# Optimization experiments

Hardware: AMD Instinct MI355X
Metric: run time of the kernel (lower is better)

## Reference

```python
import jax, jax.numpy as jnp
import numpy as np

HEADS = 16
D_MODEL = 2048
HEAD_DIM = D_MODEL // HEADS


def setup_inputs() -> dict:
    key = jax.random.key(0)
    ks = jax.random.split(key, 8)
    s = 1.0 / np.sqrt(D_MODEL)
    return {
        "hidden_states": jax.random.normal(ks[0], (2, 2048, D_MODEL), jnp.float32),
        "Wq": jax.random.normal(ks[1], (D_MODEL, D_MODEL), jnp.float32) * s,
        "bq": jax.random.normal(ks[2], (D_MODEL,), jnp.float32) * s,
        "Wk": jax.random.normal(ks[3], (D_MODEL, D_MODEL), jnp.float32) * s,
        "Wv": jax.random.normal(ks[4], (D_MODEL, D_MODEL), jnp.float32) * s,
        "bv": jax.random.normal(ks[5], (D_MODEL,), jnp.float32) * s,
        "Wo": jax.random.normal(ks[6], (D_MODEL, D_MODEL), jnp.float32) * s,
        "bo": jax.random.normal(ks[7], (D_MODEL,), jnp.float32) * s,
    }


def reference(hidden_states, Wq, bq, Wk, Wv, bv, Wo, bo):
    bsz, q_len, _ = hidden_states.shape
    # torch Linear: y = x @ W^T + b; k_W has no bias
    q = hidden_states @ Wq.T + bq
    k = hidden_states @ Wk.T
    v = hidden_states @ Wv.T + bv
    # [b, h, s, d]
    def split_heads(t):
        return t.reshape(bsz, q_len, HEADS, HEAD_DIM).transpose(0, 2, 1, 3)
    q, k, v = split_heads(q), split_heads(k), split_heads(v)
    scale = 1.0 / np.sqrt(HEAD_DIM).astype(np.float32)
    attn_weights = jnp.einsum("bhqd,bhkd->bhqk", q, k) * scale
    attn_weights = jax.nn.softmax(attn_weights, axis=-1)
    attn_output = jnp.einsum("bhqk,bhkd->bhqd", attn_weights, v)
    attn_output = attn_output.transpose(0, 2, 1, 3).reshape(bsz, q_len, D_MODEL)
    attn_output = attn_output @ Wo.T + bo
    return attn_output, attn_weights
```

## Files before the change

### kernel.cpp

```cpp
#include <hip/hip_runtime.h>

typedef _Float16 f16;
typedef _Float16 f16x4 __attribute__((ext_vector_type(4)));
typedef _Float16 f16x8 __attribute__((ext_vector_type(8)));
typedef float f32x4 __attribute__((ext_vector_type(4)));

#define DM 2048
#define NT 4096
#define SEQ 2048
#define HD 128
#define NBH 32
#define QSCALE (0.08838834764831845f * 1.4426950408889634f)

__device__ __forceinline__ void gload16(const f16* g, f16* l) {
  __builtin_amdgcn_global_load_lds(
      (const __attribute__((address_space(1))) void*)g,
      (__attribute__((address_space(3))) void*)l, 16, 0, 0);
}

__global__ __launch_bounds__(256) void cvt_f32_f16(const float* __restrict__ src,
                                                   f16* __restrict__ dst, int n4) {
  int i = blockIdx.x * 256 + threadIdx.x;
  int st = gridDim.x * 256;
  for (; i < n4; i += st) {
    float4 v = ((const float4*)src)[i];
    f16x4 h = {(f16)v.x, (f16)v.y, (f16)v.z, (f16)v.w};
    ((f16x4*)dst)[i] = h;
  }
}

__global__ __launch_bounds__(256) void cvt3_f32_f16(const float* __restrict__ s0,
                                                    const float* __restrict__ s1,
                                                    const float* __restrict__ s2,
                                                    f16* __restrict__ dst) {
  int i = blockIdx.x * 256 + threadIdx.x;
  int st = gridDim.x * 256;
  for (; i < 3 * 1048576; i += st) {
    const int r = i >> 20, j = i & 1048575;
    const float* s = (r == 0) ? s0 : ((r == 1) ? s1 : s2);
    float4 v = ((const float4*)s)[j];
    f16x4 h = {(f16)v.x, (f16)v.y, (f16)v.z, (f16)v.w};
    ((f16x4*)dst)[i] = h;
  }
}

template <int MODE>
__global__ __launch_bounds__(256, 2) void gemm_bt(const f16* __restrict__ A,
                                                  const f16* __restrict__ B,
                                                  const float* __restrict__ bias1,
                                                  const float* __restrict__ bias2,
                                                  float* __restrict__ outF,
                                                  f16* __restrict__ outQ,
                                                  f16* __restrict__ outK,
                                                  f16* __restrict__ outV) {
  __shared__ __align__(16) f16 smem[128 * 136];
  f16* const lA = smem;
  f16* const lB = smem + 8192;

  const int tid = threadIdx.x;
  const int w = tid >> 6, l = tid & 63;
  const int wr = w >> 1, wc = w & 1;

  const int nbx = gridDim.x;
  const int flat = blockIdx.y * nbx + blockIdx.x;
  const int chunk = (nbx * gridDim.y) >> 3;
  const int swz = (flat & 7) * chunk + (flat >> 3);
  const int row0 = (swz / nbx) * 128, col0 = (swz % nbx) * 128;

  f32x4 acc[4][4] = {};

  const int srow = w * 32 + (l >> 2);
  const int sk = (l & 3) * 8;
  const f16* gA = A + (size_t)(row0 + srow) * DM + sk;
  const f16* gB = B + (size_t)(col0 + srow) * DM + sk;

  {
    f16* sA = lA + w * 1024;
    f16* sB = lB + w * 1024;
    gload16(gA, sA);
    gload16(gA + 16 * DM, sA + 512);
    gload16(gB, sB);
    gload16(gB + 16 * DM, sB + 512);
  }

  int cur = 0;
  for (int k0 = 0; k0 < DM; k0 += 32) {
    __syncthreads();
    if (k0 + 32 < DM) {
      f16* sA = lA + (cur ^ 1) * 4096 + w * 1024;
      f16* sB = lB + (cur ^ 1) * 4096 + w * 1024;
      gload16(gA + k0 + 32, sA);
      gload16(gA + k0 + 32 + 16 * DM, sA + 512);
      gload16(gB + k0 + 32, sB);
      gload16(gB + k0 + 32 + 16 * DM, sB + 512);
    }
    f16x8 af[4], bf[4];
#pragma unroll
    for (int i = 0; i < 4; i++)
      af[i] = *(const f16x8*)&lA[cur * 4096 + (wr * 64 + i * 16 + (l & 15)) * 32 + (l >> 4) * 8];
#pragma unroll
    for (int i = 0; i < 4; i++)
      bf[i] = *(const f16x8*)&lB[cur * 4096 + (wc * 64 + i * 16 + (l & 15)) * 32 + (l >> 4) * 8];
#pragma unroll
    for (int mi = 0; mi < 4; mi++)
#pragma unroll
      for (int ni = 0; ni < 4; ni++)
        acc[mi][ni] = __builtin_amdgcn_mfma_f32_16x16x32_f16(af[mi], bf[ni], acc[mi][ni], 0, 0, 0);
    cur ^= 1;
  }

  const int rl0 = wr * 64 + (l >> 4) * 4;
  const int cl0 = wc * 64 + (l & 15);
  if constexpr (MODE == 0) {
#pragma unroll
    for (int mi = 0; mi < 4; mi++) {
#pragma unroll
      for (int ni = 0; ni < 4; ni++) {
        const int col = col0 + cl0 + ni * 16;
        const float bi = bias1[col];
#pragma unroll
        for (int j = 0; j < 4; j++) {
          const int row = row0 + rl0 + mi * 16 + j;
          outF[(size_t)row * DM + col] = acc[mi][ni][j] + bi;
        }
      }
    }
  } else {
    const int region = col0 >> 11;
    const int c2 = col0 & 2047;
    __syncthreads();
#pragma unroll
    for (int mi = 0; mi < 4; mi++) {
#pragma unroll
      for (int ni = 0; ni < 4; ni++) {
        const int cl = cl0 + ni * 16;
        const int cg = c2 + cl;
#pragma unroll
        for (int j = 0; j < 4; j++) {
          const int rl = rl0 + mi * 16 + j;
          const float v = acc[mi][ni][j];
          f16 hv;
          if (region == 0)
            hv = (f16)((v + bias1[cg]) * QSCALE);
          else if (region == 1)
            hv = (f16)v;
          else
            hv = (f16)(v + bias2[cg]);
          if (region == 2)
            smem[cl * 136 + rl] = hv;
          else
            smem[rl * 136 + cl] = hv;
        }
      }
    }
    __syncthreads();
    if (region == 2) {
      const int b = row0 >> 11, h = c2 >> 7, s0 = row0 & 2047;
      f16* const dst = outV + ((size_t)(b * 16 + h) * HD) * SEQ + s0;
#pragma unroll
      for (int it = 0; it < 8; it++) {
        const int ck = it * 256 + tid;
        const int rr = ck >> 4, cc = (ck & 15) * 8;
        *(f16x8*)&dst[(size_t)rr * SEQ + cc] = *(const f16x8*)&smem[rr * 136 + cc];
      }
    } else {
      f16* const dst = (region == 0 ? outQ : outK) + (size_t)row0 * DM + c2;
#pragma unroll
      for (int it = 0; it < 8; it++) {
        const int ck = it * 256 + tid;
        const int rr = ck >> 4, cc = (ck & 15) * 8;
        *(f16x8*)&dst[(size_t)rr * DM + cc] = *(const f16x8*)&smem[rr * 136 + cc];
      }
    }
  }
}

__global__ __launch_bounds__(256, 2) void attn(const f16* __restrict__ Q,
                                               const f16* __restrict__ Kt,
                                               const f16* __restrict__ Vt,
                                               float* __restrict__ Pout,
                                               f16* __restrict__ Oout) {
  __shared__ __align__(16) f16 smem[36864];
  f16* const lP = smem + 32768;

  const int tid = threadIdx.x, w = tid >> 6, l = tid & 63;
  const int t = l >> 4, sl = l & 15, t8 = l >> 3, sl8 = l & 7;

  const int flat = blockIdx.y * gridDim.x + blockIdx.x;
  const int swz = (flat & 7) * 128 + (flat >> 3);
  const int bh = swz >> 5, q0 = (swz & 31) * 64;

  const int b = bh >> 4, h = bh & 15;
  const f16* Qg = Q + (size_t)(b * SEQ) * DM + h * HD;
  const f16* Kg = Kt + (size_t)(b * SEQ) * DM + h * HD;
  const f16* Vg = Vt + (size_t)bh * HD * SEQ;

#pragma unroll
  for (int c = 0; c < 4; c++) {
    const int row = w * 16 + c * 4 + t;
    const int ch = sl ^ (row & 7);
    gload16(Qg + (size_t)(q0 + row) * DM + ch * 8, smem + 16384 + w * 2048 + c * 512);
    gload16(Kg + (size_t)row * DM + ch * 8, smem + w * 2048 + c * 512);
  }
  __syncthreads();

  f16x8 qf[4];
  {
    const int row = w * 16 + sl;
#pragma unroll
    for (int g = 0; g < 4; g++) {
      const int ch = (g * 4 + t) ^ (row & 7);
      qf[g] = *(const f16x8*)&smem[16384 + row * 128 + ch * 8];
    }
  }

  float lsum = 0.0f;

  for (int kb = 0; kb < 32; ++kb) {
    f16* const kc = smem + (kb & 1) * 8192;
    if (kb < 31) {
      f16* const kn = smem + ((kb + 1) & 1) * 8192;
#pragma unroll
      for (int c = 0; c < 4; c++) {
        const int row = w * 16 + c * 4 + t;
        const int ch = sl ^ (row & 7);
        gload16(Kg + (size_t)((kb + 1) * 64 + row) * DM + ch * 8, kn + w * 2048 + c * 512);
      }
    }
#pragma unroll
    for (int cb = 0; cb < 4; ++cb) {
      f32x4 s = {0.f, 0.f, 0.f, 0.f};
      const int key = cb * 16 + sl;
#pragma unroll
      for (int g = 0; g < 4; ++g) {
        const int ch = (g * 4 + t) ^ (key & 7);
        f16x8 kf = *(const f16x8*)&kc[key * 128 + ch * 8];
        s = __builtin_amdgcn_mfma_f32_16x16x32_f16(kf, qf[g], s, 0, 0, 0);
      }
#pragma unroll
      for (int j = 0; j < 4; j++) lsum += __builtin_amdgcn_exp2f(s[j]);
    }
    __syncthreads();
  }
  lsum += __shfl_xor(lsum, 16);
  lsum += __shfl_xor(lsum, 32);
  const float inv = 1.0f / lsum;

  {
#pragma unroll
    for (int c = 0; c < 4; c++) {
      const int row = w * 16 + c * 4 + t;
      const int ch = sl ^ (row & 7);
      gload16(Kg + (size_t)row * DM + ch * 8, smem + w * 2048 + c * 512);
    }
#pragma unroll
    for (int c = 0; c < 4; c++) {
      const int row = w * 32 + c * 8 + t8;
      const int ch = sl8 ^ (row & 7);
      gload16(Vg + (size_t)row * SEQ + ch * 8, smem + 16384 + w * 2048 + c * 512);
    }
  }
  __syncthreads();

  f32x4 oacc[8] = {};
  const int qrow = w * 16 + sl;
  float* const Prow = Pout + ((size_t)bh * SEQ + q0 + qrow) * SEQ;

  for (int kb = 0; kb < 32; ++kb) {
    f16* const kc = smem + (kb & 1) * 8192;
    f16* const vc = smem + 16384 + (kb & 1) * 8192;
    if (kb < 31) {
      f16* const kn = smem + ((kb + 1) & 1) * 8192;
      f16* const vn = smem + 16384 + ((kb + 1) & 1) * 8192;
#pragma unroll
      for (int c = 0; c < 4; c++) {
        const int row = w * 16 + c * 4 + t;
        const int ch = sl ^ (row & 7);
        gload16(Kg + (size_t)((kb + 1) * 64 + row) * DM + ch * 8, kn + w * 2048 + c * 512);
      }
#pragma unroll
      for (int c = 0; c < 4; c++) {
        const int row = w * 32 + c * 8 + t8;
        const int ch = sl8 ^ (row & 7);
        gload16(Vg + (size_t)row * SEQ + (kb + 1) * 64 + ch * 8, vn + w * 2048 + c * 512);
      }
    }
#pragma unroll
    for (int cb = 0; cb < 4; ++cb) {
      f32x4 s = {0.f, 0.f, 0.f, 0.f};
      const int key = cb * 16 + sl;
#pragma unroll
      for (int g = 0; g < 4; ++g) {
        const int ch = (g * 4 + t) ^ (key & 7);
        f16x8 kf = *(const f16x8*)&kc[key * 128 + ch * 8];
        s = __builtin_amdgcn_mfma_f32_16x16x32_f16(kf, qf[g], s, 0, 0, 0);
      }
      f32x4 p4;
      f16x4 ph;
#pragma unroll
      for (int j = 0; j < 4; j++) {
        const float p = __builtin_amdgcn_exp2f(s[j]) * inv;
        p4[j] = p;
        ph[j] = (f16)p;
      }
      __builtin_nontemporal_store(p4, (f32x4*)(Prow + kb * 64 + cb * 16 + t * 4));
      const int chs = (cb * 2 + (t >> 1)) ^ (qrow & 7);
      *(f16x4*)&lP[qrow * 64 + chs * 8 + (t & 1) * 4] = ph;
    }
    f16x8 pf[2];
#pragma unroll
    for (int ks = 0; ks < 2; ++ks) {
      const int ch = (ks * 4 + t) ^ (qrow & 7);
      pf[ks] = *(const f16x8*)&lP[qrow * 64 + ch * 8];
    }
    __builtin_amdgcn_s_setprio(1);
#pragma unroll
    for (int cb = 0; cb < 8; ++cb) {
      const int d = cb * 16 + sl;
#pragma unroll
      for (int ks = 0; ks < 2; ++ks) {
        const int ch = (ks * 4 + t) ^ (d & 7);
        f16x8 vf = *(const f16x8*)&vc[d * 64 + ch * 8];
        oacc[cb] = __builtin_amdgcn_mfma_f32_16x16x32_f16(pf[ks], vf, oacc[cb], 0, 0, 0);
      }
    }
    __builtin_amdgcn_s_setprio(0);
    __syncthreads();
  }

#pragma unroll
  for (int cb = 0; cb < 8; ++cb) {
    const int d = cb * 16 + sl;
#pragma unroll
    for (int j = 0; j < 4; j++) {
      const int lrow = w * 16 + t * 4 + j;
      Oout[((size_t)(b * SEQ + q0 + lrow)) * DM + h * HD + d] = (f16)oacc[cb][j];
    }
  }
}

extern "C" void kernel_launch(void* const* d_in, const int* in_sizes, int n_in,
                              void* d_out, int out_size, void* d_ws, size_t ws_size,
                              hipStream_t stream) {
  const float* hs = (const float*)d_in[0];
  const float* Wq = (const float*)d_in[1];
  const float* bq = (const float*)d_in[2];
  const float* Wk = (const float*)d_in[3];
  const float* Wv = (const float*)d_in[4];
  const float* bv = (const float*)d_in[5];
  const float* Wo = (const float*)d_in[6];
  const float* bo = (const float*)d_in[7];
  float* out = (float*)d_out;
  float* Pout = out + (size_t)NT * DM;

  f16* q16 = (f16*)d_ws;
  f16* k16 = q16 + (size_t)NT * DM;
  f16* vt16 = k16 + (size_t)NT * DM;
  f16* ao16 = vt16 + (size_t)NT * DM;
  f16* hs16 = (f16*)Pout;
  f16* wqkv16 = hs16 + (size_t)NT * DM;
  f16* wo16 = q16;

  cvt_f32_f16<<<2048, 256, 0, stream>>>(hs, hs16, NT * DM / 4);
  cvt3_f32_f16<<<2048, 256, 0, stream>>>(Wq, Wk, Wv, wqkv16);

  gemm_bt<3><<<dim3(6144 / 128, NT / 128), 256, 0, stream>>>(
      hs16, wqkv16, bq, bv, nullptr, q16, k16, vt16);

  attn<<<dim3(SEQ / 64, NBH), 256, 0, stream>>>(q16, k16, vt16, Pout, ao16);

  cvt_f32_f16<<<1024, 256, 0, stream>>>(Wo, wo16, DM * DM / 4);
  gemm_bt<0><<<dim3(DM / 128, NT / 128), 256, 0, stream>>>(
      ao16, wo16, bo, nullptr, out, nullptr, nullptr, nullptr);
}
```

Before: 413.7 us.

## Rewrite GEMMs as 8-wave 128x256 tiles with triple-buffered LDS pipeline

Replaces the 4-wave 128x128 GEMM with an 8-wave 128x256 tile kernel. It uses K=64 steps with a three-stage global_load_lds ring, an XOR-swizzled LDS layout to avoid bank conflicts, and explicit waitcnt, barrier and setprio scheduling that interleaves prefetch with MFMA phases. The aim is to hide global-memory latency, raise per-block reuse and cut LDS conflicts in both the QKV and output projections. In exchange it uses much more LDS (144KB per block), which may limit occupancy, and its correctness depends on hand-tuned wait counts.

Result: faster. 388.4 us (-6.1%).

```diff
diff --git a/kernel.cpp b/kernel.cpp
--- a/kernel.cpp
+++ b/kernel.cpp
@@ -17,6 +17,16 @@
       (const __attribute__((address_space(1))) void*)g,
       (__attribute__((address_space(3))) void*)l, 16, 0, 0);
 }
+
+#define LGKM0                                         \
+  asm volatile("s_waitcnt lgkmcnt(0)" ::: "memory"); \
+  __builtin_amdgcn_sched_barrier(0)
+#define VMC6                                         \
+  asm volatile("s_waitcnt vmcnt(6)" ::: "memory");   \
+  __builtin_amdgcn_sched_barrier(0)
+#define VMC0                                         \
+  asm volatile("s_waitcnt vmcnt(0)" ::: "memory");   \
+  __builtin_amdgcn_sched_barrier(0)
 
 __global__ __launch_bounds__(256) void cvt_f32_f16(const float* __restrict__ src,
                                                    f16* __restrict__ dst, int n4) {
@@ -45,72 +55,122 @@
 }
 
 template <int MODE>
-__global__ __launch_bounds__(256, 2) void gemm_bt(const f16* __restrict__ A,
-                                                  const f16* __restrict__ B,
-                                                  const float* __restrict__ bias1,
-                                                  const float* __restrict__ bias2,
-                                                  float* __restrict__ outF,
-                                                  f16* __restrict__ outQ,
-                                                  f16* __restrict__ outK,
-                                                  f16* __restrict__ outV) {
-  __shared__ __align__(16) f16 smem[128 * 136];
-  f16* const lA = smem;
-  f16* const lB = smem + 8192;
-
+__global__ __launch_bounds__(512, 2) void gemm8(const f16* __restrict__ A,
+                                                const f16* __restrict__ Bm,
+                                                const float* __restrict__ bias1,
+                                                const float* __restrict__ bias2,
+                                                float* __restrict__ outF,
+                                                f16* __restrict__ outQ,
+                                                f16* __restrict__ outK,
+                                                f16* __restrict__ outV) {
+  __shared__ __align__(16) f16 smem[73728];
   const int tid = threadIdx.x;
   const int w = tid >> 6, l = tid & 63;
-  const int wr = w >> 1, wc = w & 1;
+  const int wr = w >> 2, wc = w & 3;
+  const int sl = l & 15, t4 = l >> 4;
 
   const int nbx = gridDim.x;
   const int flat = blockIdx.y * nbx + blockIdx.x;
   const int chunk = (nbx * gridDim.y) >> 3;
   const int swz = (flat & 7) * chunk + (flat >> 3);
-  const int row0 = (swz / nbx) * 128, col0 = (swz % nbx) * 128;
+  const int row0 = (swz / nbx) * 128, col0 = (swz % nbx) * 256;
 
   f32x4 acc[4][4] = {};
 
-  const int srow = w * 32 + (l >> 2);
-  const int sk = (l & 3) * 8;
-  const f16* gA = A + (size_t)(row0 + srow) * DM + sk;
-  const f16* gB = B + (size_t)(col0 + srow) * DM + sk;
-
-  {
-    f16* sA = lA + w * 1024;
-    f16* sB = lB + w * 1024;
-    gload16(gA, sA);
-    gload16(gA + 16 * DM, sA + 512);
-    gload16(gB, sB);
-    gload16(gB + 16 * DM, sB + 512);
-  }
+  const int sr8 = l >> 3;
+  const int sch = (l & 7) ^ (sr8 & 7);
+  const f16* gA0 = A + (size_t)(row0 + w * 8 + sr8) * DM + sch * 8;
+  const f16* gB0 = Bm + (size_t)(col0 + w * 8 + sr8) * DM + sch * 8;
+
+#define SA(tb, kt, r) \
+  gload16(gA0 + (size_t)(r) * 64 * DM + (kt) * 64, smem + (tb) * 8192 + (r) * 4096 + w * 512)
+#define SB(tb, kt, r)                                  \
+  gload16(gB0 + (size_t)(r) * 64 * DM + (kt) * 64,    \
+          smem + 24576 + (tb) * 16384 + (r) * 4096 + w * 512)
+#define MF(mi, ni, av, bv) \
+  acc[mi][ni] = __builtin_amdgcn_mfma_f32_16x16x32_f16(av, bv, acc[mi][ni], 0, 0, 0)
+
+  const int sx = sl & 7;
+  const int sk0 = (t4 ^ sx) * 8;
+  const int sk1 = ((4 + t4) ^ sx) * 8;
+  const int arow = (wr * 64 + sl) * 64;
+  const int brow = (wc * 64 + sl) * 64;
+
+  SA(0, 0, 0); SA(0, 0, 1);
+  SB(0, 0, 0); SB(0, 0, 1); SB(0, 0, 2); SB(0, 0, 3);
+  SA(1, 1, 0); SA(1, 1, 1);
+  SB(1, 1, 0); SB(1, 1, 1); SB(1, 1, 2); SB(1, 1, 3);
+  VMC6;
+  __builtin_amdgcn_s_barrier();
 
   int cur = 0;
-  for (int k0 = 0; k0 < DM; k0 += 32) {
-    __syncthreads();
-    if (k0 + 32 < DM) {
-      f16* sA = lA + (cur ^ 1) * 4096 + w * 1024;
-      f16* sB = lB + (cur ^ 1) * 4096 + w * 1024;
-      gload16(gA + k0 + 32, sA);
-      gload16(gA + k0 + 32 + 16 * DM, sA + 512);
-      gload16(gB + k0 + 32, sB);
-      gload16(gB + k0 + 32 + 16 * DM, sB + 512);
-    }
-    f16x8 af[4], bf[4];
-#pragma unroll
-    for (int i = 0; i < 4; i++)
-      af[i] = *(const f16x8*)&lA[cur * 4096 + (wr * 64 + i * 16 + (l & 15)) * 32 + (l >> 4) * 8];
-#pragma unroll
-    for (int i = 0; i < 4; i++)
-      bf[i] = *(const f16x8*)&lB[cur * 4096 + (wc * 64 + i * 16 + (l & 15)) * 32 + (l >> 4) * 8];
-#pragma unroll
-    for (int mi = 0; mi < 4; mi++)
-#pragma unroll
-      for (int ni = 0; ni < 4; ni++)
-        acc[mi][ni] = __builtin_amdgcn_mfma_f32_16x16x32_f16(af[mi], bf[ni], acc[mi][ni], 0, 0, 0);
-    cur ^= 1;
-  }
-
-  const int rl0 = wr * 64 + (l >> 4) * 4;
-  const int cl0 = wc * 64 + (l & 15);
+#pragma unroll 1
+  for (int t = 0; t < 32; ++t) {
+    const int nb = (cur == 0) ? 2 : cur - 1;
+    const bool pf = (t + 2 < 32);
+    const int ab = cur * 8192;
+    const int bb = 24576 + cur * 16384;
+    f16x8 b0, b1, b2, b3, a0, a1;
+
+    b0 = *(const f16x8*)&smem[bb + brow + sk0];
+    b1 = *(const f16x8*)&smem[bb + brow + 1024 + sk0];
+    b2 = *(const f16x8*)&smem[bb + brow + 2048 + sk0];
+    b3 = *(const f16x8*)&smem[bb + brow + 3072 + sk0];
+    a0 = *(const f16x8*)&smem[ab + arow + sk0];
+    a1 = *(const f16x8*)&smem[ab + arow + 1024 + sk0];
+    if (pf) { SA(nb, t + 2, 0); SA(nb, t + 2, 1); }
+    __builtin_amdgcn_s_barrier();
+    LGKM0;
+    __builtin_amdgcn_s_setprio(1);
+    MF(0, 0, a0, b0); MF(0, 1, a0, b1); MF(0, 2, a0, b2); MF(0, 3, a0, b3);
+    MF(1, 0, a1, b0); MF(1, 1, a1, b1); MF(1, 2, a1, b2); MF(1, 3, a1, b3);
+    __builtin_amdgcn_s_setprio(0);
+    __builtin_amdgcn_s_barrier();
+
+    a0 = *(const f16x8*)&smem[ab + arow + 2048 + sk0];
+    a1 = *(const f16x8*)&smem[ab + arow + 3072 + sk0];
+    if (pf) { SB(nb, t + 2, 0); SB(nb, t + 2, 1); }
+    __builtin_amdgcn_s_barrier();
+    LGKM0;
+    __builtin_amdgcn_s_setprio(1);
+    MF(2, 0, a0, b0); MF(2, 1, a0, b1); MF(2, 2, a0, b2); MF(2, 3, a0, b3);
+    MF(3, 0, a1, b0); MF(3, 1, a1, b1); MF(3, 2, a1, b2); MF(3, 3, a1, b3);
+    __builtin_amdgcn_s_setprio(0);
+    __builtin_amdgcn_s_barrier();
+
+    b0 = *(const f16x8*)&smem[bb + brow + sk1];
+    b1 = *(const f16x8*)&smem[bb + brow + 1024 + sk1];
+    b2 = *(const f16x8*)&smem[bb + brow + 2048 + sk1];
+    b3 = *(const f16x8*)&smem[bb + brow + 3072 + sk1];
+    a0 = *(const f16x8*)&smem[ab + arow + sk1];
+    a1 = *(const f16x8*)&smem[ab + arow + 1024 + sk1];
+    if (pf) { SB(nb, t + 2, 2); SB(nb, t + 2, 3); }
+    __builtin_amdgcn_s_barrier();
+    LGKM0;
+    __builtin_amdgcn_s_setprio(1);
+    MF(0, 0, a0, b0); MF(0, 1, a0, b1); MF(0, 2, a0, b2); MF(0, 3, a0, b3);
+    MF(1, 0, a1, b0); MF(1, 1, a1, b1); MF(1, 2, a1, b2); MF(1, 3, a1, b3);
+    __builtin_amdgcn_s_setprio(0);
+    __builtin_amdgcn_s_barrier();
+
+    a0 = *(const f16x8*)&smem[ab + arow + 2048 + sk1];
+    a1 = *(const f16x8*)&smem[ab + arow + 3072 + sk1];
+    __builtin_amdgcn_s_barrier();
+    LGKM0;
+    __builtin_amdgcn_s_setprio(1);
+    MF(2, 0, a0, b0); MF(2, 1, a0, b1); MF(2, 2, a0, b2); MF(2, 3, a0, b3);
+    MF(3, 0, a1, b0); MF(3, 1, a1, b1); MF(3, 2, a1, b2); MF(3, 3, a1, b3);
+    __builtin_amdgcn_s_setprio(0);
+    if (t < 30) { VMC6; } else { VMC0; }
+    __builtin_amdgcn_s_barrier();
+    cur = (cur == 2) ? 0 : cur + 1;
+  }
+#undef SA
+#undef SB
+#undef MF
+
+  const int rl0 = wr * 64 + t4 * 4;
+  const int cl0 = wc * 64 + sl;
   if constexpr (MODE == 0) {
 #pragma unroll
     for (int mi = 0; mi < 4; mi++) {
@@ -129,47 +189,49 @@
     const int region = col0 >> 11;
     const int c2 = col0 & 2047;
     __syncthreads();
-#pragma unroll
-    for (int mi = 0; mi < 4; mi++) {
-#pragma unroll
-      for (int ni = 0; ni < 4; ni++) {
-        const int cl = cl0 + ni * 16;
-        const int cg = c2 + cl;
-#pragma unroll
-        for (int j = 0; j < 4; j++) {
-          const int rl = rl0 + mi * 16 + j;
-          const float v = acc[mi][ni][j];
-          f16 hv;
-          if (region == 0)
-            hv = (f16)((v + bias1[cg]) * QSCALE);
-          else if (region == 1)
-            hv = (f16)v;
-          else
-            hv = (f16)(v + bias2[cg]);
-          if (region == 2)
-            smem[cl * 136 + rl] = hv;
-          else
-            smem[rl * 136 + cl] = hv;
+    if (region == 2) {
+#pragma unroll
+      for (int mi = 0; mi < 4; mi++)
+#pragma unroll
+        for (int ni = 0; ni < 4; ni++) {
+          const int cl = cl0 + ni * 16;
+          const float bb2 = bias2[c2 + cl];
+#pragma unroll
+          for (int j = 0; j < 4; j++)
+            smem[cl * 136 + rl0 + mi * 16 + j] = (f16)(acc[mi][ni][j] + bb2);
         }
-      }
-    }
-    __syncthreads();
-    if (region == 2) {
-      const int b = row0 >> 11, h = c2 >> 7, s0 = row0 & 2047;
-      f16* const dst = outV + ((size_t)(b * 16 + h) * HD) * SEQ + s0;
-#pragma unroll
-      for (int it = 0; it < 8; it++) {
-        const int ck = it * 256 + tid;
-        const int rr = ck >> 4, cc = (ck & 15) * 8;
-        *(f16x8*)&dst[(size_t)rr * SEQ + cc] = *(const f16x8*)&smem[rr * 136 + cc];
+      __syncthreads();
+      const int b = row0 >> 11, s0 = row0 & 2047;
+#pragma unroll
+      for (int it = 0; it < 8; ++it) {
+        const int ck = it * 512 + tid;
+        const int ci = ck >> 4, cc = (ck & 15) * 8;
+        const int dg = c2 + ci;
+        *(f16x8*)&outV[((size_t)(b * 16 + (dg >> 7)) * HD + (dg & 127)) * SEQ + s0 + cc] =
+            *(const f16x8*)&smem[ci * 136 + cc];
       }
     } else {
+#pragma unroll
+      for (int mi = 0; mi < 4; mi++)
+#pragma unroll
+        for (int ni = 0; ni < 4; ni++) {
+          const int cl = cl0 + ni * 16;
+          const int cg = c2 + cl;
+          const float badd = (region == 0) ? bias1[cg] : 0.0f;
+#pragma unroll
+          for (int j = 0; j < 4; j++) {
+            float v = acc[mi][ni][j] + badd;
+            if (region == 0) v *= QSCALE;
+            smem[(rl0 + mi * 16 + j) * 264 + cl] = (f16)v;
+          }
+        }
+      __syncthreads();
       f16* const dst = (region == 0 ? outQ : outK) + (size_t)row0 * DM + c2;
 #pragma unroll
-      for (int it = 0; it < 8; it++) {
-        const int ck = it * 256 + tid;
-        const int rr = ck >> 4, cc = (ck & 15) * 8;
-        *(f16x8*)&dst[(size_t)rr * DM + cc] = *(const f16x8*)&smem[rr * 136 + cc];
+      for (int it = 0; it < 8; ++it) {
+        const int ck = it * 512 + tid;
+        const int rr = ck >> 5, cc = (ck & 31) * 8;
+        *(f16x8*)&dst[(size_t)rr * DM + cc] = *(const f16x8*)&smem[rr * 264 + cc];
       }
     }
   }
@@ -364,12 +426,12 @@
   cvt_f32_f16<<<2048, 256, 0, stream>>>(hs, hs16, NT * DM / 4);
   cvt3_f32_f16<<<2048, 256, 0, stream>>>(Wq, Wk, Wv, wqkv16);
 
-  gemm_bt<3><<<dim3(6144 / 128, NT / 128), 256, 0, stream>>>(
+  gemm8<3><<<dim3(6144 / 256, NT / 128), 512, 0, stream>>>(
       hs16, wqkv16, bq, bv, nullptr, q16, k16, vt16);
 
   attn<<<dim3(SEQ / 64, NBH), 256, 0, stream>>>(q16, k16, vt16, Pout, ao16);
 
   cvt_f32_f16<<<1024, 256, 0, stream>>>(Wo, wo16, DM * DM / 4);
-  gemm_bt<0><<<dim3(DM / 128, NT / 128), 256, 0, stream>>>(
+  gemm8<0><<<dim3(DM / 256, NT / 128), 512, 0, stream>>>(
       ao16, wo16, bo, nullptr, out, nullptr, nullptr, nullptr);
 }
```
